# Kernel optimization log

Hardware: AMD Instinct MI355X
Metric: run time of the kernel (lower is better)

Reference implementation:

```python
import jax, jax.numpy as jnp
import numpy as np

D_MODEL = 1024
NUM_HEADS = 16
D_K = D_MODEL // NUM_HEADS
THETA = 10000.0
MAX_SEQ_LEN = 2048
B, S = 2, 2048


def _rope(x, positions):
    """Apply interleaved RoPE. x: [B,H,S,dk], positions: [B,S]."""
    dim_idx = jnp.arange(D_K // 2, dtype=jnp.float32)
    freqs = 1.0 / (THETA ** (2.0 * dim_idx / D_K))          # [dk/2]
    angles = positions.astype(jnp.float32)[..., None] * freqs  # [B,S,dk/2]
    cos = jnp.cos(angles)[:, None, :, :]                     # [B,1,S,dk/2]
    sin = jnp.sin(angles)[:, None, :, :]
    x_even = x[..., 0::2]
    x_odd = x[..., 1::2]
    out_even = cos * x_even - sin * x_odd
    out_odd = sin * x_even + cos * x_odd
    return jnp.stack([out_even, out_odd], axis=-1).reshape(x.shape)


def setup_inputs() -> dict:
    key = jax.random.key(0)
    k1, k2, k3, k4 = jax.random.split(key, 4)
    x = jax.random.normal(k1, (B, S, D_MODEL), dtype=jnp.float32)
    token_positions = jnp.sort(
        jax.random.randint(k2, (B, S), 0, MAX_SEQ_LEN), axis=-1
    ).astype(jnp.int32)
    W_qkv = jax.random.normal(k3, (3 * D_MODEL, D_MODEL), dtype=jnp.float32) * 0.02
    W_o = jax.random.normal(k4, (D_MODEL, D_MODEL), dtype=jnp.float32) * 0.02
    return {"x": x, "token_positions": token_positions, "W_qkv": W_qkv, "W_o": W_o}


def reference(x, token_positions, W_qkv, W_o):
    # fused QKV projection: [B,S,3*D]
    qkv = jnp.einsum('bsd,ed->bse', x, W_qkv)
    qkv = qkv.reshape(B, S, 3, NUM_HEADS, D_K)
    qkv = jnp.transpose(qkv, (0, 2, 3, 1, 4))  # [B,3,H,S,dk]
    Q, K, V = qkv[:, 0], qkv[:, 1], qkv[:, 2]  # each [B,H,S,dk]

    Q = _rope(Q, token_positions)
    K = _rope(K, token_positions)

    # causal scaled dot-product attention
    scores = jnp.einsum('bhqd,bhkd->bhqk', Q, K) / jnp.sqrt(jnp.float32(D_K))
    causal = jnp.tril(jnp.ones((S, S), dtype=bool))
    scores = jnp.where(causal, scores, jnp.float32(-1e30))
    attn = jax.nn.softmax(scores, axis=-1)
    out = jnp.einsum('bhqk,bhkd->bhqd', attn, V)  # [B,H,S,dk]

    out = jnp.transpose(out, (0, 2, 1, 3)).reshape(B, S, D_MODEL)
    return jnp.einsum('bsd,ed->bse', out, W_o)
```

## Files before the change

### kernel.cpp

```cpp
#include <hip/hip_runtime.h>
#include <hip/hip_bf16.h>


using u16 = unsigned short;
typedef __attribute__((ext_vector_type(8))) short short8;
typedef __attribute__((ext_vector_type(4))) float f32x4;
typedef __attribute__((ext_vector_type(16))) float f32x16;
typedef __attribute__((ext_vector_type(2))) unsigned uint2v;
typedef __attribute__((ext_vector_type(4))) unsigned uint4v;

__device__ __forceinline__ float bf2f(u16 v) {
  unsigned u = ((unsigned)v) << 16; float f; __builtin_memcpy(&f, &u, 4); return f;
}
__device__ __forceinline__ u16 f2bf(float f) {
  unsigned u; __builtin_memcpy(&u, &f, 4);
  return (u16)((u + 0x7fffu + ((u >> 16) & 1u)) >> 16);
}
__device__ __forceinline__ float u2f(unsigned u) {
  float f; __builtin_memcpy(&f, &u, 4); return f;
}
__device__ __forceinline__ unsigned f2u(float f) {
  unsigned u; __builtin_memcpy(&u, &f, 4); return u;
}
__device__ __forceinline__ float xhalf_max(float x) {
  uint2v s = __builtin_amdgcn_permlane32_swap(f2u(x), f2u(x), false, false);
  unsigned ax = s.x, bx = s.y;
  return fmaxf(u2f(ax), u2f(bx));
}
__device__ __forceinline__ float xhalf_sum(float x) {
  uint2v s = __builtin_amdgcn_permlane32_swap(f2u(x), f2u(x), false, false);
  unsigned ax = s.x, bx = s.y;
  return u2f(ax) + u2f(bx);
}

__device__ __forceinline__ void gload_lds16(const void* g, void* l) {
  __builtin_amdgcn_global_load_lds((const __attribute__((address_space(1))) unsigned*)g,
                                   (__attribute__((address_space(3))) unsigned*)l, 16, 0, 0);
}

__global__ __launch_bounds__(256) void cvt_all(const float* __restrict__ x, const float* __restrict__ wqkv,
                                               const float* __restrict__ wo, u16* __restrict__ xb,
                                               u16* __restrict__ wqkvb, u16* __restrict__ wob) {
  int i = blockIdx.x * 256 + threadIdx.x;
  const float* src; u16* dst; int off;
  if (i < 1048576) { src = x; dst = xb; off = i; }
  else if (i < 1048576 + 786432) { src = wqkv; dst = wqkvb; off = i - 1048576; }
  else { src = wo; dst = wob; off = i - (1048576 + 786432); }
  float4 v = *(const float4*)(src + (size_t)off * 4);
  unsigned lo = f2bf(v.x) | ((unsigned)f2bf(v.y) << 16);
  unsigned hi = f2bf(v.z) | ((unsigned)f2bf(v.w) << 16);
  uint2 w; w.x = lo; w.y = hi;
  *(uint2*)(dst + (size_t)off * 4) = w;
}

template <typename OutT>
__global__ __launch_bounds__(256) void gemm_bt(const u16* __restrict__ A, const u16* __restrict__ B,
                                               OutT* __restrict__ C, int M, int N, int K) {
  __shared__ u16 As[128 * 32];
  __shared__ u16 Bs[128 * 32];
  const int tid = threadIdx.x;
  const int wave = tid >> 6;
  const int lane = tid & 63;
  const int m0 = blockIdx.x * 128;
  const int n0 = blockIdx.y * 128;
  const int wm = (wave >> 1) * 64;
  const int wn = (wave & 1) * 64;

  f32x4 acc[4][4];
#pragma unroll
  for (int m = 0; m < 4; ++m)
#pragma unroll
    for (int n = 0; n < 4; ++n) acc[m][n] = (f32x4){0.f, 0.f, 0.f, 0.f};

  const int srow = lane >> 2;
  const int scol = (lane & 3) * 8;
  const u16* Ag0 = A + (size_t)(m0 + wave * 16 + srow) * K + scol;
  const u16* Ag1 = A + (size_t)(m0 + 64 + wave * 16 + srow) * K + scol;
  const u16* Bg0 = B + (size_t)(n0 + wave * 16 + srow) * K + scol;
  const u16* Bg1 = B + (size_t)(n0 + 64 + wave * 16 + srow) * K + scol;
  u16* AsW0 = As + (wave * 16) * 32;
  u16* AsW1 = As + (64 + wave * 16) * 32;
  u16* BsW0 = Bs + (wave * 16) * 32;
  u16* BsW1 = Bs + (64 + wave * 16) * 32;

  const int fr = lane & 15;
  const int fk = (lane >> 4) * 8;

  for (int k0 = 0; k0 < K; k0 += 32) {
    __syncthreads();
    gload_lds16(Ag0 + k0, AsW0);
    gload_lds16(Ag1 + k0, AsW1);
    gload_lds16(Bg0 + k0, BsW0);
    gload_lds16(Bg1 + k0, BsW1);
    __syncthreads();

    short8 af[4], bf[4];
#pragma unroll
    for (int m = 0; m < 4; ++m)
      af[m] = *(const short8*)(As + (wm + m * 16 + fr) * 32 + fk);
#pragma unroll
    for (int n = 0; n < 4; ++n)
      bf[n] = *(const short8*)(Bs + (wn + n * 16 + fr) * 32 + fk);
#pragma unroll
    for (int m = 0; m < 4; ++m)
#pragma unroll
      for (int n = 0; n < 4; ++n)
        acc[m][n] = __builtin_amdgcn_mfma_f32_16x16x32_bf16(af[m], bf[n], acc[m][n], 0, 0, 0);
  }

  const int fg = lane >> 4;
#pragma unroll
  for (int m = 0; m < 4; ++m)
#pragma unroll
    for (int n = 0; n < 4; ++n)
#pragma unroll
      for (int r = 0; r < 4; ++r) {
        int row = m0 + wm + m * 16 + fg * 4 + r;
        int col = n0 + wn + n * 16 + fr;
        if constexpr (sizeof(OutT) == 2)
          C[(size_t)row * N + col] = (OutT)f2bf(acc[m][n][r]);
        else
          C[(size_t)row * N + col] = (OutT)acc[m][n][r];
      }
}

template <typename OutT>
__global__ __launch_bounds__(256) void gemm_bt64(const u16* __restrict__ A, const u16* __restrict__ B,
                                                 OutT* __restrict__ C, int M, int N, int K) {
  __shared__ u16 As[64 * 32];
  __shared__ u16 Bs[128 * 32];
  const int tid = threadIdx.x;
  const int wave = tid >> 6;
  const int lane = tid & 63;
  const int m0 = blockIdx.x * 64;
  const int n0 = blockIdx.y * 128;
  const int wm = (wave >> 1) * 32;
  const int wn = (wave & 1) * 64;

  f32x4 acc[2][4];
#pragma unroll
  for (int m = 0; m < 2; ++m)
#pragma unroll
    for (int n = 0; n < 4; ++n) acc[m][n] = (f32x4){0.f, 0.f, 0.f, 0.f};

  const int srow = lane >> 2;
  const int scol = (lane & 3) * 8;
  const u16* Ag = A + (size_t)(m0 + wave * 16 + srow) * K + scol;
  const u16* Bg0 = B + (size_t)(n0 + wave * 16 + srow) * K + scol;
  const u16* Bg1 = B + (size_t)(n0 + 64 + wave * 16 + srow) * K + scol;
  u16* AsW = As + (wave * 16) * 32;
  u16* BsW0 = Bs + (wave * 16) * 32;
  u16* BsW1 = Bs + (64 + wave * 16) * 32;

  const int fr = lane & 15;
  const int fk = (lane >> 4) * 8;

  for (int k0 = 0; k0 < K; k0 += 32) {
    __syncthreads();
    gload_lds16(Ag + k0, AsW);
    gload_lds16(Bg0 + k0, BsW0);
    gload_lds16(Bg1 + k0, BsW1);
    __syncthreads();

    short8 af[2], bf[4];
#pragma unroll
    for (int m = 0; m < 2; ++m)
      af[m] = *(const short8*)(As + (wm + m * 16 + fr) * 32 + fk);
#pragma unroll
    for (int n = 0; n < 4; ++n)
      bf[n] = *(const short8*)(Bs + (wn + n * 16 + fr) * 32 + fk);
#pragma unroll
    for (int m = 0; m < 2; ++m)
#pragma unroll
      for (int n = 0; n < 4; ++n)
        acc[m][n] = __builtin_amdgcn_mfma_f32_16x16x32_bf16(af[m], bf[n], acc[m][n], 0, 0, 0);
  }

  const int fg = lane >> 4;
#pragma unroll
  for (int m = 0; m < 2; ++m)
#pragma unroll
    for (int n = 0; n < 4; ++n)
#pragma unroll
      for (int r = 0; r < 4; ++r) {
        int row = m0 + wm + m * 16 + fg * 4 + r;
        int col = n0 + wn + n * 16 + fr;
        if constexpr (sizeof(OutT) == 2)
          C[(size_t)row * N + col] = (OutT)f2bf(acc[m][n][r]);
        else
          C[(size_t)row * N + col] = (OutT)acc[m][n][r];
      }
}

__global__ __launch_bounds__(256) void rope_qk(const u16* __restrict__ qkv, const int* __restrict__ pos,
                                               u16* __restrict__ Qf, u16* __restrict__ Kf) {
  int t = blockIdx.x * 256 + threadIdx.x;
  int i = t & 31;
  int h = (t >> 5) & 15;
  int s = (t >> 9) & 2047;
  int b = t >> 20;
  float p = (float)pos[(b << 11) + s];
  float ang = p * __builtin_exp2f(-(float)i * 0.41524101186f);
  float sn, cs;
  sincosf(ang, &sn, &cs);
  const u16* base = qkv + ((size_t)((b << 11) + s)) * 3072 + h * 64 + 2 * i;
  float qe = bf2f(base[0]), qo = bf2f(base[1]);
  float ke = bf2f(base[1024]), ko = bf2f(base[1025]);
  const float QS = 0.18033688011112043f;
  unsigned qw = f2bf((cs * qe - sn * qo) * QS) | ((unsigned)f2bf((sn * qe + cs * qo) * QS) << 16);
  unsigned kw = f2bf(cs * ke - sn * ko) | ((unsigned)f2bf(sn * ke + cs * ko) << 16);
  int bh = (b << 4) + h;
  int d0 = 2 * i;
  int tile = s >> 5;
  int l = (s & 31) + 32 * ((d0 >> 3) & 1);
  int j = d0 >> 4;
  int e = d0 & 7;
  size_t o = ((((size_t)bh * 64 + tile) * 4 + j) * 64 + l) * 8 + e;
  *(unsigned*)(Qf + o) = qw;
  *(unsigned*)(Kf + o) = kw;
}

__global__ __launch_bounds__(256) void v_pack(const u16* __restrict__ qkv, u16* __restrict__ Vf) {
  __shared__ u16 lds[64][72];
  const int bh = blockIdx.y;
  const int b = bh >> 4, h = bh & 15;
  const int s0 = blockIdx.x * 64;
  const int t = threadIdx.x;
  {
    const int r = t >> 3;
    const int c = t & 7;
#pragma unroll
    for (int p = 0; p < 2; ++p) {
      int s = r + p * 32;
      const u16* src = qkv + ((size_t)((b << 11) + s0 + s)) * 3072 + 2048 + h * 64 + c * 8;
      *(uint4*)&lds[s][c * 8] = *(const uint4*)src;
    }
  }
  __syncthreads();
#pragma unroll
  for (int p = 0; p < 2; ++p) {
    int item = t + p * 256;
    int tt = item >> 8;
    int seg = (item >> 6) & 3;
    int l = item & 63;
    int d = (seg >> 1) * 32 + (l & 31);
    int sb = tt * 32 + (seg & 1) * 16 + (l >> 5) * 8;
    u16 tmp[8];
#pragma unroll
    for (int e = 0; e < 8; ++e) tmp[e] = lds[sb + e][d];
    int kt = (s0 >> 5) + tt;
    size_t o = ((((size_t)bh * 64 + kt) * 4 + seg) * 64 + l) * 8;
    *(uint4*)(Vf + o) = *(uint4*)tmp;
  }
}

__global__ __launch_bounds__(256, 2) void attn6(const u16* __restrict__ Qf, const u16* __restrict__ Kf,
                                                const u16* __restrict__ Vf, u16* __restrict__ Ao) {
  __shared__ float smM[3][64], smL[3][64];
  __shared__ float smO[3][64][33];
  const int tid = threadIdx.x;
  const int lane = tid & 63;
  const int wid = tid >> 6;
  const int bid = blockIdx.x;
  const int xcd = bid & 7;
  const int rr = bid >> 3;
  const int bh = xcd * 4 + (rr & 3);
  const int qt = 63 - (rr >> 2);
  const int q0 = qt * 32;
  const u16* __restrict__ Qp = Qf + (size_t)bh * 131072;
  const u16* __restrict__ Kp = Kf + (size_t)bh * 131072;
  const u16* __restrict__ Vp = Vf + (size_t)bh * 131072;
  const int lq = lane & 31;
  const int hi = lane >> 5;

  const u16* qb = Qp + (size_t)qt * 2048 + lane * 8;
  short8 qf0 = *(const short8*)(qb);
  short8 qf1 = *(const short8*)(qb + 512);
  short8 qf2 = *(const short8*)(qb + 1024);
  short8 qf3 = *(const short8*)(qb + 1536);

  f32x16 o0, o1;
#pragma unroll
  for (int r = 0; r < 16; ++r) { o0[r] = 0.f; o1[r] = 0.f; }
  float m = -1e30f, lsum = 0.f;

  const int nkt = qt + 1;
  const int base = nkt >> 2, rem = nkt & 3;
  const int cnt = base + (wid < rem ? 1 : 0);
  const int beg = wid * base + (wid < rem ? wid : rem);

  if (cnt > 0) {
    const u16* kp = Kp + (size_t)beg * 2048 + lane * 8;
    const u16* vp = Vp + (size_t)beg * 2048 + lane * 8;
    short8 kc0 = *(const short8*)(kp);
    short8 kc1 = *(const short8*)(kp + 512);
    short8 kc2 = *(const short8*)(kp + 1024);
    short8 kc3 = *(const short8*)(kp + 1536);
    short8 vc0 = *(const short8*)(vp);
    short8 vc1 = *(const short8*)(vp + 512);
    short8 vc2 = *(const short8*)(vp + 1024);
    short8 vc3 = *(const short8*)(vp + 1536);

    for (int i = 0; i < cnt; ++i) {
      const int kt = beg + i;
      const int ktn = beg + (i + 1 < cnt ? i + 1 : i);
      const u16* kpn = Kp + (size_t)ktn * 2048 + lane * 8;
      const u16* vpn = Vp + (size_t)ktn * 2048 + lane * 8;
      short8 kn0 = *(const short8*)(kpn);
      short8 kn1 = *(const short8*)(kpn + 512);
      short8 kn2 = *(const short8*)(kpn + 1024);
      short8 kn3 = *(const short8*)(kpn + 1536);
      short8 vn0 = *(const short8*)(vpn);
      short8 vn1 = *(const short8*)(vpn + 512);
      short8 vn2 = *(const short8*)(vpn + 1024);
      short8 vn3 = *(const short8*)(vpn + 1536);

      f32x16 sc;
#pragma unroll
      for (int r = 0; r < 16; ++r) sc[r] = 0.f;
      sc = __builtin_amdgcn_mfma_f32_32x32x16_bf16(kc0, qf0, sc, 0, 0, 0);
      sc = __builtin_amdgcn_mfma_f32_32x32x16_bf16(kc1, qf1, sc, 0, 0, 0);
      sc = __builtin_amdgcn_mfma_f32_32x32x16_bf16(kc2, qf2, sc, 0, 0, 0);
      sc = __builtin_amdgcn_mfma_f32_32x32x16_bf16(kc3, qf3, sc, 0, 0, 0);

      if (kt == qt) {
#pragma unroll
        for (int r = 0; r < 16; ++r) {
          int ko = (r & 3) + 8 * (r >> 2) + 4 * hi;
          sc[r] = (ko <= lq) ? sc[r] : -1e30f;
        }
      }

      float t0 = fmaxf(fmaxf(sc[0], sc[1]), sc[2]);
      float t1 = fmaxf(fmaxf(sc[3], sc[4]), sc[5]);
      float t2 = fmaxf(fmaxf(sc[6], sc[7]), sc[8]);
      float t3 = fmaxf(fmaxf(sc[9], sc[10]), sc[11]);
      float t4 = fmaxf(fmaxf(sc[12], sc[13]), sc[14]);
      float t5 = fmaxf(fmaxf(t0, t1), sc[15]);
      float t6 = fmaxf(fmaxf(t2, t3), t4);
      float pmax = xhalf_max(fmaxf(t5, t6));

      if (!__all(pmax - m <= 11.5f)) {
        float nm = fmaxf(m, pmax);
        float alpha = __builtin_exp2f(m - nm);
        lsum *= alpha;
#pragma unroll
        for (int r = 0; r < 16; ++r) { o0[r] *= alpha; o1[r] *= alpha; }
        m = nm;
      }

#pragma unroll
      for (int r = 0; r < 16; ++r) sc[r] = __builtin_exp2f(sc[r] - m);
      float r8[8];
#pragma unroll
      for (int r = 0; r < 8; ++r) r8[r] = sc[r] + sc[r + 8];
#pragma unroll
      for (int s = 4; s >= 1; s >>= 1)
#pragma unroll
        for (int r = 0; r < s; ++r) r8[r] += r8[r + s];
      lsum += xhalf_sum(r8[0]);

      unsigned w[8];
#pragma unroll
      for (int t = 0; t < 8; ++t) {
        unsigned d;
        asm("v_cvt_pk_bf16_f32 %0, %1, %2" : "=v"(d) : "v"(sc[2 * t]), "v"(sc[2 * t + 1]));
        w[t] = d;
      }
      short8 pb0, pb1;
      {
        uint2v r1 = __builtin_amdgcn_permlane32_swap(w[0], w[2], false, false);
        uint2v r2 = __builtin_amdgcn_permlane32_swap(w[1], w[3], false, false);
        unsigned r1x = r1.x, r1y = r1.y, r2x = r2.x, r2y = r2.y;
        uint4v t4v; t4v.x = r1x; t4v.y = r2x; t4v.z = r1y; t4v.w = r2y;
        pb0 = __builtin_bit_cast(short8, t4v);
        uint2v r3 = __builtin_amdgcn_permlane32_swap(w[4], w[6], false, false);
        uint2v r4 = __builtin_amdgcn_permlane32_swap(w[5], w[7], false, false);
        unsigned r3x = r3.x, r3y = r3.y, r4x = r4.x, r4y = r4.y;
        uint4v t5v; t5v.x = r3x; t5v.y = r4x; t5v.z = r3y; t5v.w = r4y;
        pb1 = __builtin_bit_cast(short8, t5v);
      }

      o0 = __builtin_amdgcn_mfma_f32_32x32x16_bf16(vc0, pb0, o0, 0, 0, 0);
      o0 = __builtin_amdgcn_mfma_f32_32x32x16_bf16(vc1, pb1, o0, 0, 0, 0);
      o1 = __builtin_amdgcn_mfma_f32_32x32x16_bf16(vc2, pb0, o1, 0, 0, 0);
      o1 = __builtin_amdgcn_mfma_f32_32x32x16_bf16(vc3, pb1, o1, 0, 0, 0);

      kc0 = kn0; kc1 = kn1; kc2 = kn2; kc3 = kn3;
      vc0 = vn0; vc1 = vn1; vc2 = vn2; vc3 = vn3;
    }
  }

  if (wid != 0) {
    smM[wid - 1][lane] = m;
    smL[wid - 1][lane] = lsum;
#pragma unroll
    for (int r = 0; r < 16; ++r) smO[wid - 1][lane][r] = o0[r];
#pragma unroll
    for (int r = 0; r < 16; ++r) smO[wid - 1][lane][16 + r] = o1[r];
  }
  __syncthreads();
  if (wid == 0) {
    float m1 = smM[0][lane], m2 = smM[1][lane], m3 = smM[2][lane];
    float M = fmaxf(fmaxf(m, m1), fmaxf(m2, m3));
    float a0 = __builtin_exp2f(m - M);
    float a1 = __builtin_exp2f(m1 - M);
    float a2 = __builtin_exp2f(m2 - M);
    float a3 = __builtin_exp2f(m3 - M);
    float L = lsum * a0 + smL[0][lane] * a1 + smL[1][lane] * a2 + smL[2][lane] * a3;
    float inv = 1.f / L;
    const int b = bh >> 4, h = bh & 15;
    u16* outp = Ao + ((size_t)(b << 11) + q0 + lq) * 1024 + h * 64;
#pragma unroll
    for (int g = 0; g < 4; ++g) {
      int d = 8 * g + 4 * hi;
      float c[8];
#pragma unroll
      for (int j = 0; j < 4; ++j) {
        c[j] = (o0[4 * g + j] * a0 + smO[0][lane][4 * g + j] * a1 +
                smO[1][lane][4 * g + j] * a2 + smO[2][lane][4 * g + j] * a3) * inv;
        c[4 + j] = (o1[4 * g + j] * a0 + smO[0][lane][16 + 4 * g + j] * a1 +
                    smO[1][lane][16 + 4 * g + j] * a2 + smO[2][lane][16 + 4 * g + j] * a3) * inv;
      }
      uint2v w0;
      w0.x = f2bf(c[0]) | ((unsigned)f2bf(c[1]) << 16);
      w0.y = f2bf(c[2]) | ((unsigned)f2bf(c[3]) << 16);
      *(uint2v*)(outp + d) = w0;
      uint2v w1;
      w1.x = f2bf(c[4]) | ((unsigned)f2bf(c[5]) << 16);
      w1.y = f2bf(c[6]) | ((unsigned)f2bf(c[7]) << 16);
      *(uint2v*)(outp + 32 + d) = w1;
    }
  }
}

extern "C" void kernel_launch(void* const* d_in, const int* in_sizes, int n_in,
                              void* d_out, int out_size, void* d_ws, size_t ws_size,
                              hipStream_t stream) {
  const float* x = (const float*)d_in[0];
  const int* pos = (const int*)d_in[1];
  const float* Wqkv = (const float*)d_in[2];
  const float* Wo = (const float*)d_in[3];
  float* out = (float*)d_out;

  char* ws = (char*)d_ws;
  const size_t MB = 1024 * 1024;
  u16* xb     = (u16*)(ws);
  u16* wqkvb  = (u16*)(ws + 8 * MB);
  u16* wob    = (u16*)(ws + 14 * MB);
  u16* qkv    = (u16*)(ws + 16 * MB);
  u16* Qf     = (u16*)(ws + 40 * MB);
  u16* Kf     = (u16*)(ws + 48 * MB);
  u16* Vf     = (u16*)(ws + 56 * MB);
  u16* ao     = (u16*)(ws + 64 * MB);

  cvt_all<<<8192, 256, 0, stream>>>(x, Wqkv, Wo, xb, wqkvb, wob);
  gemm_bt<u16><<<dim3(32, 24), 256, 0, stream>>>(xb, wqkvb, qkv, 4096, 3072, 1024);
  rope_qk<<<8192, 256, 0, stream>>>(qkv, pos, Qf, Kf);
  v_pack<<<dim3(32, 32), 256, 0, stream>>>(qkv, Vf);
  attn6<<<2048, 256, 0, stream>>>(Qf, Kf, Vf, ao);
  gemm_bt64<float><<<dim3(64, 8), 256, 0, stream>>>(ao, wob, out, 4096, 1024, 1024);
}
```

Measured before the change: 194.7 us.

## Replace QKV GEMM with 256x256-tile, 8-wave, double-buffered pipelined kernel

```diff
diff --git a/kernel.cpp b/kernel.cpp
--- a/kernel.cpp
+++ b/kernel.cpp
@@ -53,76 +53,101 @@
   *(uint2*)(dst + (size_t)off * 4) = w;
 }
 
-template <typename OutT>
-__global__ __launch_bounds__(256) void gemm_bt(const u16* __restrict__ A, const u16* __restrict__ B,
-                                               OutT* __restrict__ C, int M, int N, int K) {
-  __shared__ u16 As[128 * 32];
-  __shared__ u16 Bs[128 * 32];
+#define HBASE(b, ab, kh) (lds + ((((b) * 2 + (ab)) * 2 + (kh)) << 13))
+#define STAGE(b, ab, kh, kt) do {                                                     \
+    const u16* _src = (ab) ? Bm : A;                                                  \
+    const int _r0 = (ab) ? n0 : m0;                                                   \
+    u16* _hb = HBASE(b, ab, kh) + (wid << 9);                                         \
+    _Pragma("unroll")                                                                 \
+    for (int _rd = 0; _rd < 2; ++_rd) {                                               \
+      int _pp = (wid << 6) + lane + _rd * 512;                                        \
+      int _r = _pp >> 2;                                                              \
+      int _ls = (_pp & 3) ^ (_r & 3);                                                 \
+      gload_lds16(_src + (size_t)(_r0 + _r) * 1024 + ((kt) << 6) + ((kh) << 5) + (_ls << 3), \
+                  _hb + _rd * 4096);                                                  \
+    } } while (0)
+#define PH(b, kk, nh, sb, sab, skh, skt, dovm) do {                                   \
+    const u16* _Ab = HBASE(b, 0, kk);                                                 \
+    const u16* _Bb = HBASE(b, 1, kk);                                                 \
+    short8 _a[8], _bv[2];                                                             \
+    _Pragma("unroll")                                                                 \
+    for (int _mf = 0; _mf < 8; ++_mf) {                                               \
+      int _r = (wr << 7) + _mf * 16 + fr;                                             \
+      _a[_mf] = *(const short8*)(_Ab + _r * 32 + ((fk ^ (_r & 3)) << 3));             \
+    }                                                                                 \
+    _Pragma("unroll")                                                                 \
+    for (int _i = 0; _i < 2; ++_i) {                                                  \
+      int _r = (wc << 6) + ((nh) * 2 + _i) * 16 + fr;                                 \
+      _bv[_i] = *(const short8*)(_Bb + _r * 32 + ((fk ^ (_r & 3)) << 3));             \
+    }                                                                                 \
+    STAGE(sb, sab, skh, skt);                                                         \
+    asm volatile("s_barrier" ::: "memory");                                           \
+    __builtin_amdgcn_s_setprio(1);                                                    \
+    _Pragma("unroll")                                                                 \
+    for (int _mf = 0; _mf < 8; ++_mf) {                                               \
+      acc[_mf][(nh) * 2 + 0] = __builtin_amdgcn_mfma_f32_16x16x32_bf16(_a[_mf], _bv[0], acc[_mf][(nh) * 2 + 0], 0, 0, 0); \
+      acc[_mf][(nh) * 2 + 1] = __builtin_amdgcn_mfma_f32_16x16x32_bf16(_a[_mf], _bv[1], acc[_mf][(nh) * 2 + 1], 0, 0, 0); \
+    }                                                                                 \
+    __builtin_amdgcn_s_setprio(0);                                                    \
+    if (dovm) asm volatile("s_waitcnt vmcnt(4)" ::: "memory");                        \
+    asm volatile("s_barrier" ::: "memory");                                           \
+  } while (0)
+
+__global__ __launch_bounds__(512, 2) void gemm_qkv_8ph(const u16* __restrict__ A,
+                                                       const u16* __restrict__ Bm,
+                                                       u16* __restrict__ C) {
+  extern __shared__ u16 lds[];
   const int tid = threadIdx.x;
-  const int wave = tid >> 6;
   const int lane = tid & 63;
-  const int m0 = blockIdx.x * 128;
-  const int n0 = blockIdx.y * 128;
-  const int wm = (wave >> 1) * 64;
-  const int wn = (wave & 1) * 64;
-
-  f32x4 acc[4][4];
-#pragma unroll
-  for (int m = 0; m < 4; ++m)
-#pragma unroll
-    for (int n = 0; n < 4; ++n) acc[m][n] = (f32x4){0.f, 0.f, 0.f, 0.f};
-
-  const int srow = lane >> 2;
-  const int scol = (lane & 3) * 8;
-  const u16* Ag0 = A + (size_t)(m0 + wave * 16 + srow) * K + scol;
-  const u16* Ag1 = A + (size_t)(m0 + 64 + wave * 16 + srow) * K + scol;
-  const u16* Bg0 = B + (size_t)(n0 + wave * 16 + srow) * K + scol;
-  const u16* Bg1 = B + (size_t)(n0 + 64 + wave * 16 + srow) * K + scol;
-  u16* AsW0 = As + (wave * 16) * 32;
-  u16* AsW1 = As + (64 + wave * 16) * 32;
-  u16* BsW0 = Bs + (wave * 16) * 32;
-  u16* BsW1 = Bs + (64 + wave * 16) * 32;
-
+  const int wid = tid >> 6;
+  const int wr = wid >> 2;
+  const int wc = wid & 3;
   const int fr = lane & 15;
-  const int fk = (lane >> 4) * 8;
-
-  for (int k0 = 0; k0 < K; k0 += 32) {
-    __syncthreads();
-    gload_lds16(Ag0 + k0, AsW0);
-    gload_lds16(Ag1 + k0, AsW1);
-    gload_lds16(Bg0 + k0, BsW0);
-    gload_lds16(Bg1 + k0, BsW1);
-    __syncthreads();
-
-    short8 af[4], bf[4];
-#pragma unroll
-    for (int m = 0; m < 4; ++m)
-      af[m] = *(const short8*)(As + (wm + m * 16 + fr) * 32 + fk);
-#pragma unroll
-    for (int n = 0; n < 4; ++n)
-      bf[n] = *(const short8*)(Bs + (wn + n * 16 + fr) * 32 + fk);
-#pragma unroll
-    for (int m = 0; m < 4; ++m)
-#pragma unroll
-      for (int n = 0; n < 4; ++n)
-        acc[m][n] = __builtin_amdgcn_mfma_f32_16x16x32_bf16(af[m], bf[n], acc[m][n], 0, 0, 0);
-  }
-
-  const int fg = lane >> 4;
-#pragma unroll
-  for (int m = 0; m < 4; ++m)
-#pragma unroll
-    for (int n = 0; n < 4; ++n)
-#pragma unroll
-      for (int r = 0; r < 4; ++r) {
-        int row = m0 + wm + m * 16 + fg * 4 + r;
-        int col = n0 + wn + n * 16 + fr;
-        if constexpr (sizeof(OutT) == 2)
-          C[(size_t)row * N + col] = (OutT)f2bf(acc[m][n][r]);
-        else
-          C[(size_t)row * N + col] = (OutT)acc[m][n][r];
-      }
-}
+  const int fk = lane >> 4;
+  const int wg = blockIdx.x;
+  const int swz = (wg & 7) * 24 + (wg >> 3);
+  const int m0 = (swz & 15) << 8;
+  const int n0 = (swz >> 4) << 8;
+
+  f32x4 acc[8][4];
+#pragma unroll
+  for (int mf = 0; mf < 8; ++mf)
+#pragma unroll
+    for (int nf = 0; nf < 4; ++nf) acc[mf][nf] = (f32x4){0.f, 0.f, 0.f, 0.f};
+
+  STAGE(0, 0, 0, 0); STAGE(0, 1, 0, 0); STAGE(0, 0, 1, 0); STAGE(0, 1, 1, 0);
+  STAGE(1, 0, 0, 1); STAGE(1, 1, 0, 1);
+  asm volatile("s_waitcnt vmcnt(4)" ::: "memory");
+  asm volatile("s_barrier" ::: "memory");
+
+  for (int n = 0; n < 8; ++n) {
+    const int ktY = 2 * n + 1;
+    int ktX2 = 2 * n + 2; if (ktX2 > 15) ktX2 = 15;
+    int ktY2 = 2 * n + 3; if (ktY2 > 15) ktY2 = 15;
+    PH(0, 0, 0, 1, 0, 1, ktY,  false);
+    PH(0, 0, 1, 1, 1, 1, ktY,  false);
+    PH(0, 1, 0, 0, 0, 0, ktX2, false);
+    PH(0, 1, 1, 0, 1, 0, ktX2, true);
+    PH(1, 0, 0, 0, 0, 1, ktX2, false);
+    PH(1, 0, 1, 0, 1, 1, ktX2, false);
+    PH(1, 1, 0, 1, 0, 0, ktY2, false);
+    PH(1, 1, 1, 1, 1, 0, ktY2, true);
+  }
+
+#pragma unroll
+  for (int mf = 0; mf < 8; ++mf)
+#pragma unroll
+    for (int nf = 0; nf < 4; ++nf)
+#pragma unroll
+      for (int j = 0; j < 4; ++j) {
+        int row = m0 + (wr << 7) + mf * 16 + fk * 4 + j;
+        int col = n0 + (wc << 6) + nf * 16 + fr;
+        C[(size_t)row * 3072 + col] = f2bf(acc[mf][nf][j]);
+      }
+}
+#undef PH
+#undef STAGE
+#undef HBASE
 
 template <typename OutT>
 __global__ __launch_bounds__(256) void gemm_bt64(const u16* __restrict__ A, const u16* __restrict__ B,
@@ -454,8 +479,11 @@
   u16* Vf     = (u16*)(ws + 56 * MB);
   u16* ao     = (u16*)(ws + 64 * MB);
 
+  (void)hipFuncSetAttribute((const void*)gemm_qkv_8ph,
+                            hipFuncAttributeMaxDynamicSharedMemorySize, 131072);
+
   cvt_all<<<8192, 256, 0, stream>>>(x, Wqkv, Wo, xb, wqkvb, wob);
-  gemm_bt<u16><<<dim3(32, 24), 256, 0, stream>>>(xb, wqkvb, qkv, 4096, 3072, 1024);
+  gemm_qkv_8ph<<<192, 512, 131072, stream>>>(xb, wqkvb, qkv);
   rope_qk<<<8192, 256, 0, stream>>>(qkv, pos, Qf, Kf);
   v_pack<<<dim3(32, 32), 256, 0, stream>>>(qkv, Vf);
   attn6<<<2048, 256, 0, stream>>>(Qf, Kf, Vf, ao);
```

Result: slower. 198.7 us (+2.1%).

## Double GEMM K-tile with XOR-swizzled LDS and vectorize RoPE packing

Applied to the files above, without the earlier changes.

```diff
diff --git a/kernel.cpp b/kernel.cpp
--- a/kernel.cpp
+++ b/kernel.cpp
@@ -54,10 +54,10 @@
 }
 
 template <typename OutT>
-__global__ __launch_bounds__(256) void gemm_bt(const u16* __restrict__ A, const u16* __restrict__ B,
-                                               OutT* __restrict__ C, int M, int N, int K) {
-  __shared__ u16 As[128 * 32];
-  __shared__ u16 Bs[128 * 32];
+__global__ __launch_bounds__(256) void gemm_bt2(const u16* __restrict__ A, const u16* __restrict__ B,
+                                                OutT* __restrict__ C, int M, int N, int K) {
+  __shared__ u16 As[128 * 64];
+  __shared__ u16 Bs[128 * 64];
   const int tid = threadIdx.x;
   const int wave = tid >> 6;
   const int lane = tid & 63;
@@ -72,40 +72,41 @@
 #pragma unroll
     for (int n = 0; n < 4; ++n) acc[m][n] = (f32x4){0.f, 0.f, 0.f, 0.f};
 
-  const int srow = lane >> 2;
-  const int scol = (lane & 3) * 8;
-  const u16* Ag0 = A + (size_t)(m0 + wave * 16 + srow) * K + scol;
-  const u16* Ag1 = A + (size_t)(m0 + 64 + wave * 16 + srow) * K + scol;
-  const u16* Bg0 = B + (size_t)(n0 + wave * 16 + srow) * K + scol;
-  const u16* Bg1 = B + (size_t)(n0 + 64 + wave * 16 + srow) * K + scol;
-  u16* AsW0 = As + (wave * 16) * 32;
-  u16* AsW1 = As + (64 + wave * 16) * 32;
-  u16* BsW0 = Bs + (wave * 16) * 32;
-  u16* BsW1 = Bs + (64 + wave * 16) * 32;
-
+  const int srow = lane >> 3;
+  const int sslot = lane & 7;
   const int fr = lane & 15;
-  const int fk = (lane >> 4) * 8;
-
-  for (int k0 = 0; k0 < K; k0 += 32) {
+  const int fk = lane >> 4;
+
+  for (int k0 = 0; k0 < K; k0 += 64) {
     __syncthreads();
-    gload_lds16(Ag0 + k0, AsW0);
-    gload_lds16(Ag1 + k0, AsW1);
-    gload_lds16(Bg0 + k0, BsW0);
-    gload_lds16(Bg1 + k0, BsW1);
+#pragma unroll
+    for (int q = 0; q < 4; ++q) {
+      int r = wave * 32 + q * 8 + srow;
+      int src_slot = sslot ^ (r & 7);
+      gload_lds16(A + (size_t)(m0 + r) * K + k0 + src_slot * 8, As + r * 64 + sslot * 8);
+      gload_lds16(B + (size_t)(n0 + r) * K + k0 + src_slot * 8, Bs + r * 64 + sslot * 8);
+    }
     __syncthreads();
 
-    short8 af[4], bf[4];
-#pragma unroll
-    for (int m = 0; m < 4; ++m)
-      af[m] = *(const short8*)(As + (wm + m * 16 + fr) * 32 + fk);
-#pragma unroll
-    for (int n = 0; n < 4; ++n)
-      bf[n] = *(const short8*)(Bs + (wn + n * 16 + fr) * 32 + fk);
-#pragma unroll
-    for (int m = 0; m < 4; ++m)
-#pragma unroll
-      for (int n = 0; n < 4; ++n)
-        acc[m][n] = __builtin_amdgcn_mfma_f32_16x16x32_bf16(af[m], bf[n], acc[m][n], 0, 0, 0);
+#pragma unroll
+    for (int kk = 0; kk < 2; ++kk) {
+      short8 af[4], bf[4];
+#pragma unroll
+      for (int m = 0; m < 4; ++m) {
+        int r = wm + m * 16 + fr;
+        af[m] = *(const short8*)(As + r * 64 + (((kk * 4 + fk) ^ (r & 7)) << 3));
+      }
+#pragma unroll
+      for (int n = 0; n < 4; ++n) {
+        int r = wn + n * 16 + fr;
+        bf[n] = *(const short8*)(Bs + r * 64 + (((kk * 4 + fk) ^ (r & 7)) << 3));
+      }
+#pragma unroll
+      for (int m = 0; m < 4; ++m)
+#pragma unroll
+        for (int n = 0; n < 4; ++n)
+          acc[m][n] = __builtin_amdgcn_mfma_f32_16x16x32_bf16(af[m], bf[n], acc[m][n], 0, 0, 0);
+    }
   }
 
   const int fg = lane >> 4;
@@ -125,10 +126,10 @@
 }
 
 template <typename OutT>
-__global__ __launch_bounds__(256) void gemm_bt64(const u16* __restrict__ A, const u16* __restrict__ B,
-                                                 OutT* __restrict__ C, int M, int N, int K) {
-  __shared__ u16 As[64 * 32];
-  __shared__ u16 Bs[128 * 32];
+__global__ __launch_bounds__(256) void gemm_bt64_2(const u16* __restrict__ A, const u16* __restrict__ B,
+                                                   OutT* __restrict__ C, int M, int N, int K) {
+  __shared__ u16 As[64 * 64];
+  __shared__ u16 Bs[128 * 64];
   const int tid = threadIdx.x;
   const int wave = tid >> 6;
   const int lane = tid & 63;
@@ -143,37 +144,46 @@
 #pragma unroll
     for (int n = 0; n < 4; ++n) acc[m][n] = (f32x4){0.f, 0.f, 0.f, 0.f};
 
-  const int srow = lane >> 2;
-  const int scol = (lane & 3) * 8;
-  const u16* Ag = A + (size_t)(m0 + wave * 16 + srow) * K + scol;
-  const u16* Bg0 = B + (size_t)(n0 + wave * 16 + srow) * K + scol;
-  const u16* Bg1 = B + (size_t)(n0 + 64 + wave * 16 + srow) * K + scol;
-  u16* AsW = As + (wave * 16) * 32;
-  u16* BsW0 = Bs + (wave * 16) * 32;
-  u16* BsW1 = Bs + (64 + wave * 16) * 32;
-
+  const int srow = lane >> 3;
+  const int sslot = lane & 7;
   const int fr = lane & 15;
-  const int fk = (lane >> 4) * 8;
-
-  for (int k0 = 0; k0 < K; k0 += 32) {
+  const int fk = lane >> 4;
+
+  for (int k0 = 0; k0 < K; k0 += 64) {
     __syncthreads();
-    gload_lds16(Ag + k0, AsW);
-    gload_lds16(Bg0 + k0, BsW0);
-    gload_lds16(Bg1 + k0, BsW1);
+#pragma unroll
+    for (int q = 0; q < 2; ++q) {
+      int r = wave * 16 + q * 8 + srow;
+      int src_slot = sslot ^ (r & 7);
+      gload_lds16(A + (size_t)(m0 + r) * K + k0 + src_slot * 8, As + r * 64 + sslot * 8);
+    }
+#pragma unroll
+    for (int q = 0; q < 4; ++q) {
+      int r = wave * 32 + q * 8 + srow;
+      int src_slot = sslot ^ (r & 7);
+      gload_lds16(B + (size_t)(n0 + r) * K + k0 + src_slot * 8, Bs + r * 64 + sslot * 8);
+    }
     __syncthreads();
 
-    short8 af[2], bf[4];
-#pragma unroll
-    for (int m = 0; m < 2; ++m)
-      af[m] = *(const short8*)(As + (wm + m * 16 + fr) * 32 + fk);
-#pragma unroll
-    for (int n = 0; n < 4; ++n)
-      bf[n] = *(const short8*)(Bs + (wn + n * 16 + fr) * 32 + fk);
-#pragma unroll
-    for (int m = 0; m < 2; ++m)
-#pragma unroll
-      for (int n = 0; n < 4; ++n)
-        acc[m][n] = __builtin_amdgcn_mfma_f32_16x16x32_bf16(af[m], bf[n], acc[m][n], 0, 0, 0);
+#pragma unroll
+    for (int kk = 0; kk < 2; ++kk) {
+      short8 af[2], bf[4];
+#pragma unroll
+      for (int m = 0; m < 2; ++m) {
+        int r = wm + m * 16 + fr;
+        af[m] = *(const short8*)(As + r * 64 + (((kk * 4 + fk) ^ (r & 7)) << 3));
+      }
+#pragma unroll
+      for (int n = 0; n < 4; ++n) {
+        int r = wn + n * 16 + fr;
+        bf[n] = *(const short8*)(Bs + r * 64 + (((kk * 4 + fk) ^ (r & 7)) << 3));
+      }
+#pragma unroll
+      for (int m = 0; m < 2; ++m)
+#pragma unroll
+        for (int n = 0; n < 4; ++n)
+          acc[m][n] = __builtin_amdgcn_mfma_f32_16x16x32_bf16(af[m], bf[n], acc[m][n], 0, 0, 0);
+    }
   }
 
   const int fg = lane >> 4;
@@ -192,32 +202,40 @@
       }
 }
 
-__global__ __launch_bounds__(256) void rope_qk(const u16* __restrict__ qkv, const int* __restrict__ pos,
-                                               u16* __restrict__ Qf, u16* __restrict__ Kf) {
+__global__ __launch_bounds__(256) void rope_qk2(const u16* __restrict__ qkv, const int* __restrict__ pos,
+                                                u16* __restrict__ Qf, u16* __restrict__ Kf) {
   int t = blockIdx.x * 256 + threadIdx.x;
-  int i = t & 31;
-  int h = (t >> 5) & 15;
-  int s = (t >> 9) & 2047;
-  int b = t >> 20;
+  int l = t & 63;
+  int j = (t >> 6) & 3;
+  int tile = (t >> 8) & 63;
+  int bh = t >> 14;
+  int b = bh >> 4, h = bh & 15;
+  int s = tile * 32 + (l & 31);
+  int dbase = j * 16 + (l >> 5) * 8;
   float p = (float)pos[(b << 11) + s];
-  float ang = p * __builtin_exp2f(-(float)i * 0.41524101186f);
-  float sn, cs;
-  sincosf(ang, &sn, &cs);
-  const u16* base = qkv + ((size_t)((b << 11) + s)) * 3072 + h * 64 + 2 * i;
-  float qe = bf2f(base[0]), qo = bf2f(base[1]);
-  float ke = bf2f(base[1024]), ko = bf2f(base[1025]);
+  const u16* src = qkv + ((size_t)((b << 11) + s)) * 3072 + h * 64 + dbase;
+  uint4 qv = *(const uint4*)src;
+  uint4 kv = *(const uint4*)(src + 1024);
+  unsigned qin[4] = {qv.x, qv.y, qv.z, qv.w};
+  unsigned kin[4] = {kv.x, kv.y, kv.z, kv.w};
+  unsigned qo[4], ko[4];
   const float QS = 0.18033688011112043f;
-  unsigned qw = f2bf((cs * qe - sn * qo) * QS) | ((unsigned)f2bf((sn * qe + cs * qo) * QS) << 16);
-  unsigned kw = f2bf(cs * ke - sn * ko) | ((unsigned)f2bf(sn * ke + cs * ko) << 16);
-  int bh = (b << 4) + h;
-  int d0 = 2 * i;
-  int tile = s >> 5;
-  int l = (s & 31) + 32 * ((d0 >> 3) & 1);
-  int j = d0 >> 4;
-  int e = d0 & 7;
-  size_t o = ((((size_t)bh * 64 + tile) * 4 + j) * 64 + l) * 8 + e;
-  *(unsigned*)(Qf + o) = qw;
-  *(unsigned*)(Kf + o) = kw;
+#pragma unroll
+  for (int kp = 0; kp < 4; ++kp) {
+    int i = (dbase >> 1) + kp;
+    float ang = p * __builtin_exp2f(-(float)i * 0.41524101186f);
+    float sn, cs;
+    sincosf(ang, &sn, &cs);
+    float qe = bf2f((u16)(qin[kp] & 0xffff)), qd = bf2f((u16)(qin[kp] >> 16));
+    float ke = bf2f((u16)(kin[kp] & 0xffff)), kd = bf2f((u16)(kin[kp] >> 16));
+    qo[kp] = f2bf((cs * qe - sn * qd) * QS) | ((unsigned)f2bf((sn * qe + cs * qd) * QS) << 16);
+    ko[kp] = f2bf(cs * ke - sn * kd) | ((unsigned)f2bf(sn * ke + cs * kd) << 16);
+  }
+  size_t o = ((((size_t)bh * 64 + tile) * 4 + j) * 64 + l) * 8;
+  uint4 qw; qw.x = qo[0]; qw.y = qo[1]; qw.z = qo[2]; qw.w = qo[3];
+  uint4 kw; kw.x = ko[0]; kw.y = ko[1]; kw.z = ko[2]; kw.w = ko[3];
+  *(uint4*)(Qf + o) = qw;
+  *(uint4*)(Kf + o) = kw;
 }
 
 __global__ __launch_bounds__(256) void v_pack(const u16* __restrict__ qkv, u16* __restrict__ Vf) {
@@ -455,9 +473,9 @@
   u16* ao     = (u16*)(ws + 64 * MB);
 
   cvt_all<<<8192, 256, 0, stream>>>(x, Wqkv, Wo, xb, wqkvb, wob);
-  gemm_bt<u16><<<dim3(32, 24), 256, 0, stream>>>(xb, wqkvb, qkv, 4096, 3072, 1024);
-  rope_qk<<<8192, 256, 0, stream>>>(qkv, pos, Qf, Kf);
+  gemm_bt2<u16><<<dim3(32, 24), 256, 0, stream>>>(xb, wqkvb, qkv, 4096, 3072, 1024);
+  rope_qk2<<<2048, 256, 0, stream>>>(qkv, pos, Qf, Kf);
   v_pack<<<dim3(32, 32), 256, 0, stream>>>(qkv, Vf);
   attn6<<<2048, 256, 0, stream>>>(Qf, Kf, Vf, ao);
-  gemm_bt64<float><<<dim3(64, 8), 256, 0, stream>>>(ao, wob, out, 4096, 1024, 1024);
-}
+  gemm_bt64_2<float><<<dim3(64, 8), 256, 0, stream>>>(ao, wob, out, 4096, 1024, 1024);
+}
```

Result: faster. 179.3 us (-7.9%).
